# Kernel tuning notes

Measured on AMD Instinct MI355X. Metric: run time of the kernel, lower is better.

Reference implementation:

```python
import jax, jax.numpy as jnp
import numpy as np

N = 100000   # num_entities
R = 8        # num_relations
B = 8        # num_bases = min(R, 30)
D = 128      # hidden_dim == embedding_dim
E = 800000   # num_edges


def rgcn_layer(x, edge_index, edge_type, basis, comp, root, bias):
    """PyG-style RGCNConv with basis decomposition and per-relation mean aggregation.

    Mean aggregation is linear, so we aggregate raw source features per
    (dst, relation) segment first, then apply the relation transform once
    per (node, relation) instead of per edge.
    """
    n, r = x.shape[0], comp.shape[0]
    W = jnp.einsum('rb,bio->rio', comp, basis)          # [R, D_in, D_out]
    src, dst = edge_index[0], edge_index[1]
    seg = dst * r + edge_type                            # segment key per edge
    agg = jax.ops.segment_sum(x[src], seg, num_segments=n * r)          # [N*R, D_in]
    cnt = jax.ops.segment_sum(jnp.ones((src.shape[0],), x.dtype), seg,
                              num_segments=n * r)                        # [N*R]
    agg = (agg / jnp.maximum(cnt, 1.0)[:, None]).reshape(n, r, -1)       # [N, R, D_in]
    return jnp.einsum('nri,rio->no', agg, W) + x @ root + bias


def setup_inputs() -> dict:
    key = jax.random.key(0)
    ks = jax.random.split(key, 12)
    s_in = 1.0 / np.sqrt(D)
    inp = {
        'edge_index': jax.random.randint(ks[0], (2, E), 0, N, dtype=jnp.int64 if jax.config.jax_enable_x64 else jnp.int32),
        'edge_type': jax.random.randint(ks[1], (E,), 0, R, dtype=jnp.int64 if jax.config.jax_enable_x64 else jnp.int32),
        'emb': jax.random.normal(ks[2], (N, D), jnp.float32) * s_in,
        'basis1': jax.random.normal(ks[3], (B, D, D), jnp.float32) * s_in,
        'comp1': jax.random.normal(ks[4], (R, B), jnp.float32) * (1.0 / np.sqrt(B)),
        'root1': jax.random.normal(ks[5], (D, D), jnp.float32) * s_in,
        'bias1': jnp.zeros((D,), jnp.float32),
        'basis2': jax.random.normal(ks[6], (B, D, D), jnp.float32) * s_in,
        'comp2': jax.random.normal(ks[7], (R, B), jnp.float32) * (1.0 / np.sqrt(B)),
        'root2': jax.random.normal(ks[8], (D, D), jnp.float32) * s_in,
        'bias2': jnp.zeros((D,), jnp.float32),
    }
    return inp


def reference(edge_index, edge_type, emb, basis1, comp1, root1, bias1,
              basis2, comp2, root2, bias2):
    # layer 1 + ReLU (dropout is identity at eval time)
    x = rgcn_layer(emb, edge_index, edge_type, basis1, comp1, root1, bias1)
    x = jax.nn.relu(x)
    # layer 2 (output layer, no activation)
    x = rgcn_layer(x, edge_index, edge_type, basis2, comp2, root2, bias2)
    return x
```

## Files before the change

kernel.cpp:

```cpp
#include <hip/hip_runtime.h>

#define NN 100000
#define RR 8
#define BB 8
#define DD 128
#define EE 800000
#define KT 1152
#define NBLK 782
#define NSEG2 (NBLK * 1024)
#define AGSTR 132
#define NCVT 6250
#define NCNT 3125
#define NPB  576

typedef __attribute__((ext_vector_type(8))) __bf16 bf16x8;
typedef __attribute__((ext_vector_type(4))) float f32x4;
typedef __attribute__((ext_vector_type(4))) unsigned int u32x4;

__device__ __forceinline__ unsigned short f2bf(float f) {
    unsigned u = __float_as_uint(f);
    u += 0x7fffu + ((u >> 16) & 1u);
    return (unsigned short)(u >> 16);
}
__device__ __forceinline__ float bf2f(unsigned short h) {
    return __uint_as_float(((unsigned)h) << 16);
}

__device__ __forceinline__ void prepB_body(int idx,
                                           const float* __restrict__ root,
                                           const float* __restrict__ comp,
                                           const float* __restrict__ basis,
                                           unsigned short* __restrict__ Bhi,
                                           unsigned short* __restrict__ Blo) {
    if (idx >= DD * KT) return;
    int o = idx / KT, k = idx - o * KT;
    float v;
    if (k < DD) {
        v = root[k * DD + o];
    } else {
        int r = (k - DD) >> 7, i = (k - DD) & 127;
        float s = 0.f;
#pragma unroll
        for (int b = 0; b < BB; ++b)
            s += comp[r * BB + b] * basis[((size_t)b * DD + i) * DD + o];
        v = s;
    }
    unsigned short hi = f2bf(v);
    Bhi[idx] = hi;
    Blo[idx] = f2bf(v - bf2f(hi));
}

__global__ __launch_bounds__(256) void k_pre(
    const float* __restrict__ x, unsigned short* __restrict__ xh,
    const int* __restrict__ ei, const int* __restrict__ et, int* __restrict__ cnt,
    const float* __restrict__ root1, const float* __restrict__ comp1,
    const float* __restrict__ basis1,
    unsigned short* __restrict__ Bhi1, unsigned short* __restrict__ Blo1,
    const float* __restrict__ root2, const float* __restrict__ comp2,
    const float* __restrict__ basis2,
    unsigned short* __restrict__ Bhi2, unsigned short* __restrict__ Blo2)
{
    const int blk = blockIdx.x, tid = threadIdx.x;
    if (blk < NCVT) {
        int i = blk * 256 + tid;
        f32x4 a = ((const f32x4*)x)[2 * i];
        f32x4 b = ((const f32x4*)x)[2 * i + 1];
        u32x4 o;
        o[0] = (unsigned)f2bf(a[0]) | ((unsigned)f2bf(a[1]) << 16);
        o[1] = (unsigned)f2bf(a[2]) | ((unsigned)f2bf(a[3]) << 16);
        o[2] = (unsigned)f2bf(b[0]) | ((unsigned)f2bf(b[1]) << 16);
        o[3] = (unsigned)f2bf(b[2]) | ((unsigned)f2bf(b[3]) << 16);
        ((u32x4*)xh)[i] = o;
    } else if (blk < NCVT + NCNT) {
        int e = (blk - NCVT) * 256 + tid;
        if (e < EE) {
            int d = ei[EE + e];
            atomicAdd(&cnt[(d >> 7) * 1024 + et[e] * 128 + (d & 127)], 1);
        }
    } else if (blk < NCVT + NCNT + NPB) {
        prepB_body((blk - NCVT - NCNT) * 256 + tid, root1, comp1, basis1, Bhi1, Blo1);
    } else {
        prepB_body((blk - NCVT - NCNT - NPB) * 256 + tid, root2, comp2, basis2, Bhi2, Blo2);
    }
}

__global__ __launch_bounds__(256) void k_scan_local(const int* __restrict__ cnt,
                                                    int* __restrict__ loc,
                                                    int* __restrict__ bsum) {
    __shared__ int tmp[256];
    int t = threadIdx.x, i = blockIdx.x * 256 + t;
    int v = cnt[i];
    tmp[t] = v; __syncthreads();
    int val = v;
#pragma unroll
    for (int d = 1; d < 256; d <<= 1) {
        int a = (t >= d) ? tmp[t - d] : 0;
        __syncthreads();
        val += a; tmp[t] = val;
        __syncthreads();
    }
    loc[i] = val - v;
    if (t == 255) bsum[blockIdx.x] = val;
}

__global__ void k_scan_bsum(const int* __restrict__ bsum, int* __restrict__ boff) {
    __shared__ int tmp[256];
    const int NB = NSEG2 / 256;
    const int CH = 13;
    int t = threadIdx.x;
    int base = t * CH, s = 0;
    for (int j = 0; j < CH; ++j) { int idx = base + j; if (idx < NB) s += bsum[idx]; }
    tmp[t] = s; __syncthreads();
    int val = s;
#pragma unroll
    for (int d = 1; d < 256; d <<= 1) {
        int a = (t >= d) ? tmp[t - d] : 0;
        __syncthreads();
        val += a; tmp[t] = val;
        __syncthreads();
    }
    int run = val - s;
    for (int j = 0; j < CH; ++j) { int idx = base + j; if (idx < NB) { boff[idx] = run; run += bsum[idx]; } }
}

__global__ __launch_bounds__(256) void k_scan_add(int* __restrict__ loc,
                                                  const int* __restrict__ boff) {
    int i = blockIdx.x * 256 + threadIdx.x;
    loc[i] += boff[i >> 8];
}

__global__ __launch_bounds__(256) void k_scatter(const int* __restrict__ ei,
                                                 const int* __restrict__ et,
                                                 int* __restrict__ segoff,
                                                 int* __restrict__ spk) {
    int e = blockIdx.x * 256 + threadIdx.x;
    if (e < EE) {
        int d = ei[EE + e];
        int key = (d >> 7) * 1024 + et[e] * 128 + (d & 127);
        int pos = atomicAdd(&segoff[key], 1);
        spk[pos] = ei[e];
    }
}

template <bool WRITE_H1>
__global__ __launch_bounds__(256, 3) void k_gemm(
    const unsigned short* __restrict__ xh,
    const unsigned short* __restrict__ Bhi,
    const unsigned short* __restrict__ Blo,
    const float* __restrict__ bias,
    const int* __restrict__ spk,
    const int* __restrict__ segend,
    unsigned short* __restrict__ h1h,
    float* __restrict__ outf)
{
    __shared__ unsigned short Aagg[128 * AGSTR];
    __shared__ unsigned short Bhs[128 * 32];
    __shared__ unsigned short Bls[128 * 32];
    __shared__ unsigned short sbeg16[1026];

    const int tid = threadIdx.x;
    const int b = blockIdx.x;
    const int M0 = b * 128;
    const int gbase = b * 1024;

    const int beg0 = (gbase == 0) ? 0 : segend[gbase - 1];
    for (int i = tid; i < 1025; i += 256) {
        int v = (gbase + i == 0) ? 0 : segend[gbase + i - 1];
        sbeg16[i] = (unsigned short)(v - beg0);
    }

    const int wave = tid >> 6, lane = tid & 63;
    const int quad = lane >> 4, lm = lane & 15;
    const int node = tid >> 1, half = tid & 1;

    f32x4 acc[2][8];
#pragma unroll
    for (int a = 0; a < 2; ++a)
#pragma unroll
        for (int n = 0; n < 8; ++n) acc[a][n] = (f32x4){0.f, 0.f, 0.f, 0.f};

    const int bro = tid >> 2;
    const int bq = tid & 3;
    const int bsw = bq ^ ((bro >> 1) & 3);
    const int brd = lm * 32 + (quad ^ ((lm >> 1) & 3)) * 8;
    u32x4 bh0, bh1, bl0, bl1;

    auto bload = [&](int k0) {
        bh0 = *(const u32x4*)(Bhi + (size_t)bro * KT + k0 + bq * 8);
        bl0 = *(const u32x4*)(Blo + (size_t)bro * KT + k0 + bq * 8);
        bh1 = *(const u32x4*)(Bhi + (size_t)(64 + bro) * KT + k0 + bq * 8);
        bl1 = *(const u32x4*)(Blo + (size_t)(64 + bro) * KT + k0 + bq * 8);
    };
    auto bwrite = [&]() {
        *(u32x4*)&Bhs[bro * 32 + bsw * 8] = bh0;
        *(u32x4*)&Bls[bro * 32 + bsw * 8] = bl0;
        *(u32x4*)&Bhs[(64 + bro) * 32 + bsw * 8] = bh1;
        *(u32x4*)&Bls[(64 + bro) * 32 + bsw * 8] = bl1;
    };

    auto kstep = [&](bf16x8 af0, bf16x8 af1, int k0next, bool tail) {
#pragma unroll
        for (int nt = 0; nt < 8; ++nt) {
            bf16x8 bh = __builtin_bit_cast(bf16x8, *(const u32x4*)&Bhs[nt * 512 + brd]);
            bf16x8 bl = __builtin_bit_cast(bf16x8, *(const u32x4*)&Bls[nt * 512 + brd]);
            acc[0][nt] = __builtin_amdgcn_mfma_f32_16x16x32_bf16(af0, bh, acc[0][nt], 0, 0, 0);
            acc[0][nt] = __builtin_amdgcn_mfma_f32_16x16x32_bf16(af0, bl, acc[0][nt], 0, 0, 0);
            acc[1][nt] = __builtin_amdgcn_mfma_f32_16x16x32_bf16(af1, bh, acc[1][nt], 0, 0, 0);
            acc[1][nt] = __builtin_amdgcn_mfma_f32_16x16x32_bf16(af1, bl, acc[1][nt], 0, 0, 0);
        }
        if (tail) return;
        __syncthreads();
        bwrite();
        if (k0next >= 0) bload(k0next);
        __syncthreads();
    };

    bload(0);
    bwrite();
    bload(32);

    int r0 = M0 + wave * 32 + lm;      if (r0 > NN - 1) r0 = NN - 1;
    int r1 = M0 + wave * 32 + 16 + lm; if (r1 > NN - 1) r1 = NN - 1;
    const unsigned short* pa0 = xh + (size_t)r0 * DD + quad * 8;
    const unsigned short* pa1 = xh + (size_t)r1 * DD + quad * 8;

    __syncthreads();

#pragma unroll
    for (int ks = 0; ks < 4; ++ks) {
        bf16x8 af0 = __builtin_bit_cast(bf16x8, *(const u32x4*)(pa0 + ks * 32));
        bf16x8 af1 = __builtin_bit_cast(bf16x8, *(const u32x4*)(pa1 + ks * 32));
        const int k0n = (ks < 2) ? (ks + 2) * 32 : DD + (ks - 2) * 32;
        kstep(af0, af1, k0n, false);
    }

    for (int r = 0; r < RR; ++r) {
        const int si = r * 128 + node;
        const int rel = (int)sbeg16[si];
        const int beg = beg0 + rel;
        const int cs = (int)sbeg16[si + 1] - rel;

#pragma unroll
        for (int p = 0; p < 2; ++p) {
            const int coff = half * 64 + p * 32;
            float vlo[16], vhi[16];
#pragma unroll
            for (int j = 0; j < 16; ++j) { vlo[j] = 0.f; vhi[j] = 0.f; }

            for (int t = 0; t < cs; ++t) {
                const int sp = spk[beg + t];
                const u32x4* ps = (const u32x4*)(xh + (size_t)sp * DD + coff);
                u32x4 a0 = ps[0], a1 = ps[1], a2 = ps[2], a3 = ps[3];
#pragma unroll
                for (int w = 0; w < 4; ++w) {
                    vlo[w]      += __uint_as_float(a0[w] << 16);
                    vhi[w]      += __uint_as_float(a0[w] & 0xFFFF0000u);
                    vlo[4 + w]  += __uint_as_float(a1[w] << 16);
                    vhi[4 + w]  += __uint_as_float(a1[w] & 0xFFFF0000u);
                    vlo[8 + w]  += __uint_as_float(a2[w] << 16);
                    vhi[8 + w]  += __uint_as_float(a2[w] & 0xFFFF0000u);
                    vlo[12 + w] += __uint_as_float(a3[w] << 16);
                    vhi[12 + w] += __uint_as_float(a3[w] & 0xFFFF0000u);
                }
            }

            const float inv = 1.0f / (float)(cs > 1 ? cs : 1);
            unsigned pk[16];
#pragma unroll
            for (int j = 0; j < 16; ++j)
                pk[j] = (unsigned)f2bf(vlo[j] * inv) | ((unsigned)f2bf(vhi[j] * inv) << 16);
            unsigned short* pw = &Aagg[node * AGSTR + coff];
            *(u32x4*)(pw + 0)  = (u32x4){pk[0],  pk[1],  pk[2],  pk[3]};
            *(u32x4*)(pw + 8)  = (u32x4){pk[4],  pk[5],  pk[6],  pk[7]};
            *(u32x4*)(pw + 16) = (u32x4){pk[8],  pk[9],  pk[10], pk[11]};
            *(u32x4*)(pw + 24) = (u32x4){pk[12], pk[13], pk[14], pk[15]};
        }

        __syncthreads();

#pragma unroll
        for (int s = 0; s < 4; ++s) {
            bf16x8 af0 = __builtin_bit_cast(bf16x8,
                *(const u32x4*)&Aagg[(wave * 32 + lm) * AGSTR + s * 32 + quad * 8]);
            bf16x8 af1 = __builtin_bit_cast(bf16x8,
                *(const u32x4*)&Aagg[(wave * 32 + 16 + lm) * AGSTR + s * 32 + quad * 8]);
            const bool tail = (r == RR - 1) && (s == 3);
            const int k0n = (s < 2) ? DD + r * 128 + (s + 2) * 32
                          : ((r < RR - 1) ? DD + (r + 1) * 128 + (s - 2) * 32 : -1);
            kstep(af0, af1, k0n, tail);
        }
    }

#pragma unroll
    for (int mt = 0; mt < 2; ++mt) {
#pragma unroll
        for (int nt = 0; nt < 8; ++nt) {
            const float bvn = bias[nt * 16 + lm];
#pragma unroll
            for (int rg = 0; rg < 4; ++rg) {
                int row = M0 + wave * 32 + mt * 16 + quad * 4 + rg;
                if (row < NN) {
                    int col = nt * 16 + lm;
                    float v = acc[mt][nt][rg] + bvn;
                    if (WRITE_H1) h1h[(size_t)row * DD + col] = f2bf(fmaxf(v, 0.f));
                    else          outf[(size_t)row * DD + col] = v;
                }
            }
        }
    }
}


extern "C" void kernel_launch(void* const* d_in, const int* in_sizes, int n_in,
                              void* d_out, int out_size, void* d_ws, size_t ws_size,
                              hipStream_t stream) {
    const int*   ei     = (const int*)d_in[0];
    const int*   et     = (const int*)d_in[1];
    const float* emb    = (const float*)d_in[2];
    const float* basis1 = (const float*)d_in[3];
    const float* comp1  = (const float*)d_in[4];
    const float* root1  = (const float*)d_in[5];
    const float* bias1  = (const float*)d_in[6];
    const float* basis2 = (const float*)d_in[7];
    const float* comp2  = (const float*)d_in[8];
    const float* root2  = (const float*)d_in[9];
    const float* bias2  = (const float*)d_in[10];
    float* out = (float*)d_out;
    (void)in_sizes; (void)n_in; (void)out_size; (void)ws_size;

    char* ws = (char*)d_ws;
    int*            cnt    = (int*)(ws + 0);
    int*            segoff = (int*)(ws + 3203072);
    int*            spk    = (int*)(ws + 6406144);
    int*            bsum   = (int*)(ws + 9606144);
    int*            boff   = (int*)(ws + 9618656);
    unsigned short* Bhi1   = (unsigned short*)(ws + 9656320);
    unsigned short* Blo1   = (unsigned short*)(ws + 9951232);
    unsigned short* Bhi2   = (unsigned short*)(ws + 10246144);
    unsigned short* Blo2   = (unsigned short*)(ws + 10541056);
    unsigned short* embh   = (unsigned short*)(ws + 10835968);
    unsigned short* h1h    = (unsigned short*)(ws + 36435968);

    hipMemsetAsync(cnt, 0, (size_t)NSEG2 * 4, stream);

    k_pre<<<NCVT + NCNT + 2 * NPB, 256, 0, stream>>>(
        emb, embh, ei, et, cnt,
        root1, comp1, basis1, Bhi1, Blo1,
        root2, comp2, basis2, Bhi2, Blo2);

    k_scan_local<<<NSEG2 / 256, 256, 0, stream>>>(cnt, segoff, bsum);
    k_scan_bsum <<<1, 256, 0, stream>>>(bsum, boff);
    k_scan_add  <<<NSEG2 / 256, 256, 0, stream>>>(segoff, boff);
    k_scatter   <<<(EE + 255) / 256, 256, 0, stream>>>(ei, et, segoff, spk);

    k_gemm<true> <<<NBLK, 256, 0, stream>>>(embh, Bhi1, Blo1, bias1, spk, segoff, h1h, nullptr);
    k_gemm<false><<<NBLK, 256, 0, stream>>>(h1h,  Bhi2, Blo2, bias2, spk, segoff, nullptr, out);
}
```

Before: 542.7 us.

## Halve GEMM row tile to 64 nodes and split waves over N

Shrinks the per-block node tile from 128 to 64 rows, doubling the grid, and re-keys the segment layout to match (512 segments per block). The four waves now split the tile as 2 (M) by 2 (N), so each wave holds half the accumulators. Each thread gathers a 32-column slice instead of two 64-column halves, and occupancy is raised to 4 blocks per CU. This targets load balance and latency hiding in the gather-heavy phase, at the cost of reloading the full B matrix twice as often across blocks.

New measurement: 484.4 us. -10.7%, faster.

```diff
diff --git a/kernel.cpp b/kernel.cpp
--- a/kernel.cpp
+++ b/kernel.cpp
@@ -6,8 +6,10 @@
 #define DD 128
 #define EE 800000
 #define KT 1152
-#define NBLK 782
-#define NSEG2 (NBLK * 1024)
+#define BM 64
+#define NBLK 1563
+#define SEGPB 512
+#define NSEG2 (NBLK * SEGPB)
 #define AGSTR 132
 #define NCVT 6250
 #define NCNT 3125
@@ -75,7 +77,7 @@
         int e = (blk - NCVT) * 256 + tid;
         if (e < EE) {
             int d = ei[EE + e];
-            atomicAdd(&cnt[(d >> 7) * 1024 + et[e] * 128 + (d & 127)], 1);
+            atomicAdd(&cnt[(d >> 6) * SEGPB + et[e] * BM + (d & 63)], 1);
         }
     } else if (blk < NCVT + NCNT + NPB) {
         prepB_body((blk - NCVT - NCNT) * 256 + tid, root1, comp1, basis1, Bhi1, Blo1);
@@ -136,14 +138,14 @@
     int e = blockIdx.x * 256 + threadIdx.x;
     if (e < EE) {
         int d = ei[EE + e];
-        int key = (d >> 7) * 1024 + et[e] * 128 + (d & 127);
+        int key = (d >> 6) * SEGPB + et[e] * BM + (d & 63);
         int pos = atomicAdd(&segoff[key], 1);
         spk[pos] = ei[e];
     }
 }
 
 template <bool WRITE_H1>
-__global__ __launch_bounds__(256, 3) void k_gemm(
+__global__ __launch_bounds__(256, 4) void k_gemm(
     const unsigned short* __restrict__ xh,
     const unsigned short* __restrict__ Bhi,
     const unsigned short* __restrict__ Blo,
@@ -153,31 +155,32 @@
     unsigned short* __restrict__ h1h,
     float* __restrict__ outf)
 {
-    __shared__ unsigned short Aagg[128 * AGSTR];
+    __shared__ unsigned short Aagg[BM * AGSTR];
     __shared__ unsigned short Bhs[128 * 32];
     __shared__ unsigned short Bls[128 * 32];
-    __shared__ unsigned short sbeg16[1026];
+    __shared__ unsigned short sbeg16[SEGPB + 2];
 
     const int tid = threadIdx.x;
     const int b = blockIdx.x;
-    const int M0 = b * 128;
-    const int gbase = b * 1024;
+    const int M0 = b * BM;
+    const int gbase = b * SEGPB;
 
     const int beg0 = (gbase == 0) ? 0 : segend[gbase - 1];
-    for (int i = tid; i < 1025; i += 256) {
+    for (int i = tid; i < SEGPB + 1; i += 256) {
         int v = (gbase + i == 0) ? 0 : segend[gbase + i - 1];
         sbeg16[i] = (unsigned short)(v - beg0);
     }
 
     const int wave = tid >> 6, lane = tid & 63;
     const int quad = lane >> 4, lm = lane & 15;
-    const int node = tid >> 1, half = tid & 1;
-
-    f32x4 acc[2][8];
+    const int mh = wave & 1, nh = wave >> 1;
+    const int node = tid >> 2, cslice = tid & 3;
+
+    f32x4 acc[2][4];
 #pragma unroll
     for (int a = 0; a < 2; ++a)
 #pragma unroll
-        for (int n = 0; n < 8; ++n) acc[a][n] = (f32x4){0.f, 0.f, 0.f, 0.f};
+        for (int n = 0; n < 4; ++n) acc[a][n] = (f32x4){0.f, 0.f, 0.f, 0.f};
 
     const int bro = tid >> 2;
     const int bq = tid & 3;
@@ -200,13 +203,14 @@
 
     auto kstep = [&](bf16x8 af0, bf16x8 af1, int k0next, bool tail) {
 #pragma unroll
-        for (int nt = 0; nt < 8; ++nt) {
+        for (int j = 0; j < 4; ++j) {
+            const int nt = nh * 4 + j;
             bf16x8 bh = __builtin_bit_cast(bf16x8, *(const u32x4*)&Bhs[nt * 512 + brd]);
             bf16x8 bl = __builtin_bit_cast(bf16x8, *(const u32x4*)&Bls[nt * 512 + brd]);
-            acc[0][nt] = __builtin_amdgcn_mfma_f32_16x16x32_bf16(af0, bh, acc[0][nt], 0, 0, 0);
-            acc[0][nt] = __builtin_amdgcn_mfma_f32_16x16x32_bf16(af0, bl, acc[0][nt], 0, 0, 0);
-            acc[1][nt] = __builtin_amdgcn_mfma_f32_16x16x32_bf16(af1, bh, acc[1][nt], 0, 0, 0);
-            acc[1][nt] = __builtin_amdgcn_mfma_f32_16x16x32_bf16(af1, bl, acc[1][nt], 0, 0, 0);
+            acc[0][j] = __builtin_amdgcn_mfma_f32_16x16x32_bf16(af0, bh, acc[0][j], 0, 0, 0);
+            acc[0][j] = __builtin_amdgcn_mfma_f32_16x16x32_bf16(af0, bl, acc[0][j], 0, 0, 0);
+            acc[1][j] = __builtin_amdgcn_mfma_f32_16x16x32_bf16(af1, bh, acc[1][j], 0, 0, 0);
+            acc[1][j] = __builtin_amdgcn_mfma_f32_16x16x32_bf16(af1, bl, acc[1][j], 0, 0, 0);
         }
         if (tail) return;
         __syncthreads();
@@ -219,8 +223,8 @@
     bwrite();
     bload(32);
 
-    int r0 = M0 + wave * 32 + lm;      if (r0 > NN - 1) r0 = NN - 1;
-    int r1 = M0 + wave * 32 + 16 + lm; if (r1 > NN - 1) r1 = NN - 1;
+    int r0 = M0 + mh * 32 + lm;      if (r0 > NN - 1) r0 = NN - 1;
+    int r1 = M0 + mh * 32 + 16 + lm; if (r1 > NN - 1) r1 = NN - 1;
     const unsigned short* pa0 = xh + (size_t)r0 * DD + quad * 8;
     const unsigned short* pa1 = xh + (size_t)r1 * DD + quad * 8;
 
@@ -235,14 +239,13 @@
     }
 
     for (int r = 0; r < RR; ++r) {
-        const int si = r * 128 + node;
-        const int rel = (int)sbeg16[si];
-        const int beg = beg0 + rel;
-        const int cs = (int)sbeg16[si + 1] - rel;
-
-#pragma unroll
-        for (int p = 0; p < 2; ++p) {
-            const int coff = half * 64 + p * 32;
+        const int si = r * BM + node;
+        const int rel0 = (int)sbeg16[si];
+        const int beg = beg0 + rel0;
+        const int cs = (int)sbeg16[si + 1] - rel0;
+
+        const int coff = cslice * 32;
+        {
             float vlo[16], vhi[16];
 #pragma unroll
             for (int j = 0; j < 16; ++j) { vlo[j] = 0.f; vhi[j] = 0.f; }
@@ -281,9 +284,9 @@
 #pragma unroll
         for (int s = 0; s < 4; ++s) {
             bf16x8 af0 = __builtin_bit_cast(bf16x8,
-                *(const u32x4*)&Aagg[(wave * 32 + lm) * AGSTR + s * 32 + quad * 8]);
+                *(const u32x4*)&Aagg[(mh * 32 + lm) * AGSTR + s * 32 + quad * 8]);
             bf16x8 af1 = __builtin_bit_cast(bf16x8,
-                *(const u32x4*)&Aagg[(wave * 32 + 16 + lm) * AGSTR + s * 32 + quad * 8]);
+                *(const u32x4*)&Aagg[(mh * 32 + 16 + lm) * AGSTR + s * 32 + quad * 8]);
             const bool tail = (r == RR - 1) && (s == 3);
             const int k0n = (s < 2) ? DD + r * 128 + (s + 2) * 32
                           : ((r < RR - 1) ? DD + (r + 1) * 128 + (s - 2) * 32 : -1);
@@ -294,14 +297,15 @@
 #pragma unroll
     for (int mt = 0; mt < 2; ++mt) {
 #pragma unroll
-        for (int nt = 0; nt < 8; ++nt) {
+        for (int j = 0; j < 4; ++j) {
+            const int nt = nh * 4 + j;
             const float bvn = bias[nt * 16 + lm];
 #pragma unroll
             for (int rg = 0; rg < 4; ++rg) {
-                int row = M0 + wave * 32 + mt * 16 + quad * 4 + rg;
+                int row = M0 + mh * 32 + mt * 16 + quad * 4 + rg;
                 if (row < NN) {
                     int col = nt * 16 + lm;
-                    float v = acc[mt][nt][rg] + bvn;
+                    float v = acc[mt][j][rg] + bvn;
                     if (WRITE_H1) h1h[(size_t)row * DD + col] = f2bf(fmaxf(v, 0.f));
                     else          outf[(size_t)row * DD + col] = v;
                 }
```
